# Kernel tuning notes

Hardware: AMD Instinct MI355X
Metric: run time of the kernel (lower is better)

The kernel has to match this reference:

```python
import jax, jax.numpy as jnp
import numpy as np

HIDDEN = 2048
N_HEADS = 16
N_KV_HEADS = 4
HEAD_DIM = HIDDEN // N_HEADS  # 128
ROPE_THETA = 10000.0
BATCH = 2
SEQ = 2048


def setup_inputs() -> dict:
    key = jax.random.key(0)
    k1, k2, k3, k4, k5 = jax.random.split(key, 5)
    s = 0.02
    return {
        "hidden_states": jax.random.normal(k1, (BATCH, SEQ, HIDDEN), dtype=jnp.float32),
        "attention_mask": jnp.zeros((BATCH, 1, 1, SEQ), dtype=jnp.float32),
        "Wq": jax.random.normal(k2, (HIDDEN, N_HEADS * HEAD_DIM), dtype=jnp.float32) * s,
        "Wk": jax.random.normal(k3, (HIDDEN, N_KV_HEADS * HEAD_DIM), dtype=jnp.float32) * s,
        "Wv": jax.random.normal(k4, (HIDDEN, N_KV_HEADS * HEAD_DIM), dtype=jnp.float32) * s,
        "Wo": jax.random.normal(k5, (N_HEADS * HEAD_DIM, HIDDEN), dtype=jnp.float32) * s,
    }


def _rope_cos_sin(seq_len, dtype):
    inv_freq = 1.0 / (ROPE_THETA ** (jnp.arange(0, HEAD_DIM, 2, dtype=jnp.float32) / HEAD_DIM))
    t = jnp.arange(seq_len, dtype=jnp.float32)
    freqs = t[:, None] * inv_freq[None, :]            # [S, D/2]
    emb = jnp.concatenate([freqs, freqs], axis=-1)    # [S, D]
    cos = jnp.cos(emb)[None, None, :, :].astype(dtype)  # [1,1,S,D]
    sin = jnp.sin(emb)[None, None, :, :].astype(dtype)
    return cos, sin


def _apply_rope(x, cos, sin):
    # x: [B,H,S,D]; faithful to torch code: rotated = cat((-x[...,1::2], x[...,::2]), -1)
    x1 = x[..., ::2]
    x2 = x[..., 1::2]
    rotated = jnp.concatenate([-x2, x1], axis=-1)
    return x * cos + rotated * sin


def reference(hidden_states, attention_mask, Wq, Wk, Wv, Wo):
    B, S, _ = hidden_states.shape
    scale = HEAD_DIM ** -0.5

    q = (hidden_states @ Wq).reshape(B, S, N_HEADS, HEAD_DIM).transpose(0, 2, 1, 3)      # [B,H,S,D]
    k = (hidden_states @ Wk).reshape(B, S, N_KV_HEADS, HEAD_DIM).transpose(0, 2, 1, 3)   # [B,KV,S,D]
    v = (hidden_states @ Wv).reshape(B, S, N_KV_HEADS, HEAD_DIM).transpose(0, 2, 1, 3)

    cos, sin = _rope_cos_sin(S, hidden_states.dtype)
    q = _apply_rope(q, cos, sin)
    k = _apply_rope(k, cos, sin)

    rep = N_HEADS // N_KV_HEADS
    k = jnp.repeat(k, rep, axis=1)  # [B,H,S,D]
    v = jnp.repeat(v, rep, axis=1)

    scores = jnp.einsum("bhqd,bhkd->bhqk", q, k) * scale  # [B,H,S,S]
    causal = jnp.tril(jnp.ones((S, S), dtype=bool))[None, None]
    scores = jnp.where(causal, scores, -jnp.inf)
    scores = scores + attention_mask  # additive float mask, broadcast [B,1,1,S]

    attn = jax.nn.softmax(scores, axis=-1)
    out = jnp.einsum("bhqk,bhkd->bhqd", attn, v)           # [B,H,S,D]
    out = out.transpose(0, 2, 1, 3).reshape(B, S, N_HEADS * HEAD_DIM)
    return out @ Wo
```

## Files before the change

### kernel.cpp

```cpp
#include <hip/hip_runtime.h>
#include <hip/hip_bf16.h>

#define BATCH 2
#define SEQ   2048
#define NH    16
#define NKV   4
#define HD    128
#define KDIM  2048
#define MROWS 4096
#define NQKV  3072

typedef __attribute__((ext_vector_type(8))) short  s16x8;
typedef __attribute__((ext_vector_type(4))) short  s16x4;
typedef __attribute__((ext_vector_type(4))) float  f32x4;
typedef __attribute__((ext_vector_type(8))) __bf16 b16x8;

__device__ __forceinline__ unsigned short f2bf(float f) {
  __hip_bfloat16 h = __float2bfloat16(f);
  return *reinterpret_cast<unsigned short*>(&h);
}
__device__ __forceinline__ float bf2f(unsigned short h) {
  union { unsigned int u; float f; } x; x.u = ((unsigned int)h) << 16;
  return x.f;
}

__device__ __forceinline__ f32x4 MFMA16(s16x8 a, s16x8 b, f32x4 c) {
  return __builtin_amdgcn_mfma_f32_16x16x32_bf16(
      __builtin_bit_cast(b16x8, a), __builtin_bit_cast(b16x8, b), c, 0, 0, 0);
}

__device__ __forceinline__ void gload_lds16(const void* g, void* lds) {
  __builtin_amdgcn_global_load_lds(
      (const __attribute__((address_space(1))) void*)g,
      (__attribute__((address_space(3))) void*)lds, 16, 0, 0);
}

__global__ __launch_bounds__(256) void transpose_convert(
    const float* __restrict__ W, unsigned short* __restrict__ WT, int Kd, int Nd) {
  __shared__ float tile[32][33];
  int n0 = blockIdx.x * 32, k0 = blockIdx.y * 32;
  int tx = threadIdx.x & 31, ty = threadIdx.x >> 5;
#pragma unroll
  for (int i = 0; i < 4; ++i)
    tile[ty + i * 8][tx] = W[(size_t)(k0 + ty + i * 8) * Nd + n0 + tx];
  __syncthreads();
#pragma unroll
  for (int i = 0; i < 4; ++i)
    WT[(size_t)(n0 + ty + i * 8) * Kd + k0 + tx] = f2bf(tile[tx][ty + i * 8]);
}

__global__ __launch_bounds__(256) void conv_bf16(
    const float* __restrict__ X, unsigned short* __restrict__ Y) {
  int i = blockIdx.x * 256 + threadIdx.x;
  const float4 a = ((const float4*)X)[2 * i];
  const float4 b = ((const float4*)X)[2 * i + 1];
  s16x8 o;
  o[0] = (short)f2bf(a.x); o[1] = (short)f2bf(a.y);
  o[2] = (short)f2bf(a.z); o[3] = (short)f2bf(a.w);
  o[4] = (short)f2bf(b.x); o[5] = (short)f2bf(b.y);
  o[6] = (short)f2bf(b.z); o[7] = (short)f2bf(b.w);
  ((s16x8*)Y)[i] = o;
}

__global__ __launch_bounds__(256) void rope_table_kernel(float* __restrict__ tbl) {
  int i = blockIdx.x * 256 + threadIdx.x;
  int s = i >> 6, j = i & 63;
  float inv = powf(10000.0f, -(float)(2 * j) * (1.0f / 128.0f));
  float f = (float)s * inv;
  tbl[2 * i]     = cosf(f);
  tbl[2 * i + 1] = sinf(f);
}

__global__ __launch_bounds__(256) void gemm_qkv(
    const unsigned short* __restrict__ A, const unsigned short* __restrict__ BT,
    unsigned short* __restrict__ Qo, unsigned short* __restrict__ Ko,
    unsigned short* __restrict__ Vo) {
  __shared__ __align__(16) unsigned short la[128][32];
  __shared__ __align__(16) unsigned short lb[128][32];
  int tid = threadIdx.x, lane = tid & 63, w = tid >> 6;
  int m0 = blockIdx.y * 128, n0 = blockIdx.x * 128;
  int wr = (w >> 1) * 64, wc = (w & 1) * 64;
  int fr = lane & 15, kg = (lane >> 4) * 8, rg = (lane >> 4) * 4;
  f32x4 acc[4][4] = {};
  for (int kt = 0; kt < KDIM; kt += 32) {
    __syncthreads();
#pragma unroll
    for (int i = 0; i < 2; ++i) {
      int idx = tid + i * 256;
      int row = idx >> 2, seg = idx & 3;
      gload_lds16(A + (size_t)(m0 + row) * KDIM + kt + seg * 8,
                  (char*)la + (size_t)(i * 256 + w * 64) * 16);
      gload_lds16(BT + (size_t)(n0 + row) * KDIM + kt + seg * 8,
                  (char*)lb + (size_t)(i * 256 + w * 64) * 16);
    }
    __syncthreads();
    s16x8 af[4], bf[4];
#pragma unroll
    for (int mi = 0; mi < 4; ++mi) af[mi] = *(const s16x8*)(&la[wr + mi * 16 + fr][kg]);
#pragma unroll
    for (int ni = 0; ni < 4; ++ni) bf[ni] = *(const s16x8*)(&lb[wc + ni * 16 + fr][kg]);
#pragma unroll
    for (int mi = 0; mi < 4; ++mi)
#pragma unroll
      for (int ni = 0; ni < 4; ++ni) acc[mi][ni] = MFMA16(af[mi], bf[ni], acc[mi][ni]);
  }
  int rbase = m0 + wr + rg;
#pragma unroll
  for (int ni = 0; ni < 4; ++ni) {
    int gn = n0 + wc + ni * 16 + fr;
    if (gn < 2048) {
      int hh = gn >> 7, d = gn & 127;
#pragma unroll
      for (int mi = 0; mi < 4; ++mi)
#pragma unroll
        for (int r = 0; r < 4; ++r) {
          int grow = rbase + mi * 16 + r;
          int bb = grow >> 11, ss = grow & 2047;
          Qo[((size_t)(bb * NH + hh) * SEQ + ss) * HD + d] = f2bf(acc[mi][ni][r]);
        }
    } else if (gn < 2560) {
      int c = gn - 2048, kvh = c >> 7, d = c & 127;
#pragma unroll
      for (int mi = 0; mi < 4; ++mi)
#pragma unroll
        for (int r = 0; r < 4; ++r) {
          int grow = rbase + mi * 16 + r;
          int bb = grow >> 11, ss = grow & 2047;
          Ko[((size_t)(bb * NKV + kvh) * SEQ + ss) * HD + d] = f2bf(acc[mi][ni][r]);
        }
    } else {
      int c = gn - 2560, kvh = c >> 7, d = c & 127;
#pragma unroll
      for (int mi = 0; mi < 4; ++mi) {
        int grow0 = rbase + mi * 16;
        int bb = grow0 >> 11, ss = grow0 & 2047;
        s16x4 pk;
#pragma unroll
        for (int r = 0; r < 4; ++r) pk[r] = (short)f2bf(acc[mi][ni][r]);
        *(s16x4*)(Vo + ((size_t)(bb * NKV + kvh) * HD + d) * SEQ + ss) = pk;
      }
    }
  }
}

__global__ __launch_bounds__(256) void gemm_out(
    const unsigned short* __restrict__ A, const unsigned short* __restrict__ BT,
    float* __restrict__ C) {
  __shared__ __align__(16) unsigned short la[128][32];
  __shared__ __align__(16) unsigned short lb[128][32];
  int tid = threadIdx.x, lane = tid & 63, w = tid >> 6;
  int m0 = blockIdx.y * 128, n0 = blockIdx.x * 128;
  int wr = (w >> 1) * 64, wc = (w & 1) * 64;
  int fr = lane & 15, kg = (lane >> 4) * 8, rg = (lane >> 4) * 4;
  f32x4 acc[4][4] = {};
  for (int kt = 0; kt < KDIM; kt += 32) {
    __syncthreads();
#pragma unroll
    for (int i = 0; i < 2; ++i) {
      int idx = tid + i * 256;
      int row = idx >> 2, seg = idx & 3;
      gload_lds16(A + (size_t)(m0 + row) * KDIM + kt + seg * 8,
                  (char*)la + (size_t)(i * 256 + w * 64) * 16);
      gload_lds16(BT + (size_t)(n0 + row) * KDIM + kt + seg * 8,
                  (char*)lb + (size_t)(i * 256 + w * 64) * 16);
    }
    __syncthreads();
    s16x8 af[4], bf[4];
#pragma unroll
    for (int mi = 0; mi < 4; ++mi) af[mi] = *(const s16x8*)(&la[wr + mi * 16 + fr][kg]);
#pragma unroll
    for (int ni = 0; ni < 4; ++ni) bf[ni] = *(const s16x8*)(&lb[wc + ni * 16 + fr][kg]);
#pragma unroll
    for (int mi = 0; mi < 4; ++mi)
#pragma unroll
      for (int ni = 0; ni < 4; ++ni) acc[mi][ni] = MFMA16(af[mi], bf[ni], acc[mi][ni]);
  }
  int rbase = m0 + wr + rg;
#pragma unroll
  for (int ni = 0; ni < 4; ++ni) {
    int gn = n0 + wc + ni * 16 + fr;
#pragma unroll
    for (int mi = 0; mi < 4; ++mi)
#pragma unroll
      for (int r = 0; r < 4; ++r)
        C[(size_t)(rbase + mi * 16 + r) * 2048 + gn] = acc[mi][ni][r];
  }
}

__global__ __launch_bounds__(256) void rope2(
    unsigned short* __restrict__ X, const float* __restrict__ tbl) {
  __shared__ __align__(16) unsigned short xs[32][136];
  int tid = threadIdx.x;
  size_t r0 = (size_t)blockIdx.x * 32;
#pragma unroll
  for (int i = 0; i < 2; ++i) {
    int idx = tid + i * 256;
    int pr = idx >> 4, seg = idx & 15;
    *(s16x8*)(&xs[pr][seg * 8]) = *(const s16x8*)(X + (r0 + pr) * 128 + seg * 8);
  }
  __syncthreads();
  int pr = tid >> 3, jb = (tid & 7) * 8;
  size_t row = r0 + pr;
  int s = (int)(row & (SEQ - 1));
  s16x8 o0, o1;
#pragma unroll
  for (int j0 = 0; j0 < 8; ++j0) {
    int j = jb + j0;
    float c  = tbl[(s * 64 + j) * 2];
    float sn = tbl[(s * 64 + j) * 2 + 1];
    float xj   = bf2f(xs[pr][j]);
    float xj64 = bf2f(xs[pr][j + 64]);
    float x2j  = bf2f(xs[pr][2 * j]);
    float x2j1 = bf2f(xs[pr][2 * j + 1]);
    o0[j0] = (short)f2bf(xj * c - x2j1 * sn);
    o1[j0] = (short)f2bf(xj64 * c + x2j * sn);
  }
  unsigned short* xp = X + row * 128;
  *(s16x8*)(xp + jb)      = o0;
  *(s16x8*)(xp + 64 + jb) = o1;
}

__global__ __launch_bounds__(512, 2) void attn_fwd(
    const unsigned short* __restrict__ Q, const unsigned short* __restrict__ K,
    const unsigned short* __restrict__ VT, const float* __restrict__ mask,
    unsigned short* __restrict__ O) {
  __shared__ __align__(16) unsigned short kt_[2][64][136];
  __shared__ __align__(16) unsigned short vt_[128][68];
  __shared__ __align__(16) unsigned short pt_[8][16][36];

  int tid = threadIdx.x, lane = tid & 63, w = tid >> 6;
  int l = blockIdx.x;
  int grp = l & 7, slot = l >> 3;
  int hloc = slot & 3, p = slot >> 2;
  int b = grp >> 2, kvh = grp & 3, h = kvh * 4 + hloc;
  int half = w >> 2, wsub = w & 3;
  int qt = half ? p : 31 - p;
  int qw = qt * 64 + wsub * 16;
  int fr = lane & 15, g = lane >> 4, kg = g * 8, rg = g * 4;

  const unsigned short* Qb = Q + (size_t)(b * NH + h) * SEQ * HD;
  const unsigned short* Kb = K + (size_t)(b * NKV + kvh) * SEQ * HD;
  const unsigned short* Vb = VT + (size_t)(b * NKV + kvh) * HD * SEQ;
  const float* mb = mask + (size_t)b * SEQ;

  int krow = tid >> 4, kpos = (tid & 15) * 8;
  int vrow = tid >> 3, vcol = (tid & 7) * 8;

  const float sc2 = 0.12751744584812722f;
  const float L2E = 1.44269504088896f;
  int bS = b * SEQ;
  int ntiles = 32 - p;

  s16x8 aq[4];
#pragma unroll
  for (int dc = 0; dc < 4; ++dc)
    aq[dc] = *(const s16x8*)(Qb + (size_t)(qw + fr) * HD + dc * 32 + kg);

  f32x4 oacc[8] = {};
  float m_r = -3e38f, l_r = 0.f;

  s16x8 kreg[2], vreg[2];
  kreg[0] = *(const s16x8*)(Kb + (size_t)krow * HD + kpos);
  kreg[1] = *(const s16x8*)(Kb + (size_t)(krow + 32) * HD + kpos);
  vreg[0] = *(const s16x8*)(Vb + (size_t)vrow * SEQ + vcol);
  vreg[1] = *(const s16x8*)(Vb + (size_t)(vrow + 64) * SEQ + vcol);
  *(s16x8*)(&kt_[0][krow][kpos])      = kreg[0];
  *(s16x8*)(&kt_[0][krow + 32][kpos]) = kreg[1];
  __syncthreads();

  int cur = 0;
  for (int t = 0; t < ntiles; ++t) {
    int kv0 = t * 64;
    bool notlast = (t + 1 < ntiles);
    bool active = (kv0 <= qw + 15);
    bool diag   = (kv0 + 63 > qw);

    *(s16x8*)(&vt_[vrow][vcol])      = vreg[0];
    *(s16x8*)(&vt_[vrow + 64][vcol]) = vreg[1];
    if (notlast) {
      kreg[0] = *(const s16x8*)(Kb + (size_t)(kv0 + 64 + krow) * HD + kpos);
      kreg[1] = *(const s16x8*)(Kb + (size_t)(kv0 + 96 + krow) * HD + kpos);
    }

    f32x4 sf[4];
    if (active) {
      __builtin_amdgcn_s_setprio(1);
#pragma unroll
      for (int mk = 0; mk < 4; ++mk) {
        s16x8 ak[4];
#pragma unroll
        for (int dc = 0; dc < 4; ++dc)
          ak[dc] = *(const s16x8*)(&kt_[cur][mk * 16 + fr][dc * 32 + kg]);
        sf[mk] = f32x4{0.f, 0.f, 0.f, 0.f};
#pragma unroll
        for (int dc = 0; dc < 4; ++dc)
          sf[mk] = MFMA16(ak[dc], aq[dc], sf[mk]);
      }
      __builtin_amdgcn_s_setprio(0);

#pragma unroll
      for (int mk = 0; mk < 4; ++mk) {
        float4 mv = *(const float4*)(mb + kv0 + mk * 16 + rg);
        float mvr[4] = {mv.x * L2E, mv.y * L2E, mv.z * L2E, mv.w * L2E};
        if (diag) {
#pragma unroll
          for (int r = 0; r < 4; ++r) {
            int kv = kv0 + mk * 16 + rg + r;
            float v = sf[mk][r] * sc2 + mvr[r];
            sf[mk][r] = (kv <= qw + fr) ? v : -3e38f;
          }
        } else {
#pragma unroll
          for (int r = 0; r < 4; ++r)
            sf[mk][r] = sf[mk][r] * sc2 + mvr[r];
        }
      }

      float pm = -3e38f;
#pragma unroll
      for (int mk = 0; mk < 4; ++mk)
#pragma unroll
        for (int r = 0; r < 4; ++r) pm = fmaxf(pm, sf[mk][r]);
      pm = fmaxf(pm, __shfl_xor(pm, 16, 64));
      pm = fmaxf(pm, __shfl_xor(pm, 32, 64));
      if (!__all(pm - m_r <= 8.0f)) {
        float mo = m_r;
        float mn = fmaxf(mo, pm);
        float al = exp2f(mo - mn);
        m_r = mn;
        l_r *= al;
#pragma unroll
        for (int r = 0; r < 4; ++r) {
          float ar = __shfl(al, rg + r, 16);
#pragma unroll
          for (int od = 0; od < 8; ++od) oacc[od][r] *= ar;
        }
      }
      float rs = 0.f;
#pragma unroll
      for (int mk = 0; mk < 4; ++mk)
#pragma unroll
        for (int r = 0; r < 4; ++r) {
          float ppv = exp2f(sf[mk][r] - m_r);
          sf[mk][r] = ppv;
          rs += ppv;
        }
      rs += __shfl_xor(rs, 16, 64);
      rs += __shfl_xor(rs, 32, 64);
      l_r += rs;
    }

    if (notlast) {
      *(s16x8*)(&kt_[cur ^ 1][krow][kpos])      = kreg[0];
      *(s16x8*)(&kt_[cur ^ 1][krow + 32][kpos]) = kreg[1];
    }
    __syncthreads();

    if (notlast) {
      vreg[0] = *(const s16x8*)(Vb + (size_t)vrow * SEQ + kv0 + 64 + vcol);
      vreg[1] = *(const s16x8*)(Vb + (size_t)(vrow + 64) * SEQ + kv0 + 64 + vcol);
    }

    if (active) {
#pragma unroll
      for (int kk = 0; kk < 2; ++kk) {
#pragma unroll
        for (int mh = 0; mh < 2; ++mh) {
          int mk = kk * 2 + mh;
          s16x4 pk;
#pragma unroll
          for (int r = 0; r < 4; ++r) pk[r] = (short)f2bf(sf[mk][r]);
          *(s16x4*)(&pt_[w][fr][mh * 16 + rg]) = pk;
        }
        s16x8 ap = *(const s16x8*)(&pt_[w][fr][kg]);
        __builtin_amdgcn_s_setprio(1);
#pragma unroll
        for (int od = 0; od < 8; ++od) {
          s16x8 bv = *(const s16x8*)(&vt_[od * 16 + fr][kk * 32 + kg]);
          oacc[od] = MFMA16(ap, bv, oacc[od]);
        }
        __builtin_amdgcn_s_setprio(0);
      }
    }
    __syncthreads();
    cur ^= 1;
  }

  float iv = 1.0f / l_r;
  float ivr[4];
#pragma unroll
  for (int r = 0; r < 4; ++r) ivr[r] = __shfl(iv, rg + r, 16);
#pragma unroll
  for (int r = 0; r < 4; ++r) {
    unsigned short* op = O + (size_t)(bS + qw + rg + r) * 2048 + h * 128 + fr;
#pragma unroll
    for (int od = 0; od < 8; ++od)
      op[od * 16] = f2bf(oacc[od][r] * ivr[r]);
  }
}

extern "C" void kernel_launch(void* const* d_in, const int* in_sizes, int n_in,
                              void* d_out, int out_size, void* d_ws, size_t ws_size,
                              hipStream_t stream) {
  const float* hidden = (const float*)d_in[0];
  const float* mask   = (const float*)d_in[1];
  const float* Wq     = (const float*)d_in[2];
  const float* Wk     = (const float*)d_in[3];
  const float* Wv     = (const float*)d_in[4];
  const float* Wo     = (const float*)d_in[5];
  float* out = (float*)d_out;

  char* ws = (char*)d_ws;
  unsigned short* BT  = (unsigned short*)(ws);
  unsigned short* WoT = (unsigned short*)(ws + 12582912);
  unsigned short* Qb  = (unsigned short*)(ws + 20971520);
  unsigned short* Kb  = (unsigned short*)(ws + 37748736);
  unsigned short* VT  = (unsigned short*)(ws + 41943040);
  unsigned short* AO  = (unsigned short*)(ws + 46137344);
  float*          tbl = (float*)(ws + 62914560);
  unsigned short* Ab  = AO;

  conv_bf16<<<MROWS * KDIM / (256 * 8), 256, 0, stream>>>(hidden, Ab);
  transpose_convert<<<dim3(64, 64), 256, 0, stream>>>(Wq, BT, KDIM, 2048);
  transpose_convert<<<dim3(16, 64), 256, 0, stream>>>(Wk, BT + (size_t)2048 * KDIM, KDIM, 512);
  transpose_convert<<<dim3(16, 64), 256, 0, stream>>>(Wv, BT + (size_t)2560 * KDIM, KDIM, 512);
  transpose_convert<<<dim3(64, 64), 256, 0, stream>>>(Wo, WoT, KDIM, 2048);
  rope_table_kernel<<<512, 256, 0, stream>>>(tbl);

  gemm_qkv<<<dim3(NQKV / 128, MROWS / 128), 256, 0, stream>>>(Ab, BT, Qb, Kb, VT);
  rope2<<<(BATCH * NH * SEQ) / 32, 256, 0, stream>>>(Qb, tbl);
  rope2<<<(BATCH * NKV * SEQ) / 32, 256, 0, stream>>>(Kb, tbl);
  attn_fwd<<<dim3(512), 512, 0, stream>>>(Qb, Kb, VT, mask, AO);
  gemm_out<<<dim3(2048 / 128, MROWS / 128), 256, 0, stream>>>(AO, WoT, out);
}
```

Measured before the change: 229.8 us.

## Swizzle GEMM block order, use LDS-only barriers, tree-reduce row max

Both GEMMs now launch on a 1D grid and remap block indices with an XCD-aware swizzle, so consecutive blocks on the same XCD work on nearby tiles and share L2. The attention kernel replaces __syncthreads with a barrier that waits only for LDS counters, so outstanding global prefetch loads of K/V need not drain at each barrier. The row-max reduction becomes a balanced tree to shorten the dependency chain. These are three separate changes; if the barrier ordering assumption is wrong, the weaker barrier could cause a race.

Result: no change. 230.9 us (+0.5%).

```diff
diff --git a/kernel.cpp b/kernel.cpp
--- a/kernel.cpp
+++ b/kernel.cpp
@@ -14,6 +14,11 @@
 typedef __attribute__((ext_vector_type(4))) short  s16x4;
 typedef __attribute__((ext_vector_type(4))) float  f32x4;
 typedef __attribute__((ext_vector_type(8))) __bf16 b16x8;
+
+#define BARRIER_LDS() do { \
+    asm volatile("s_waitcnt lgkmcnt(0)" ::: "memory"); \
+    __builtin_amdgcn_s_barrier(); \
+  } while (0)
 
 __device__ __forceinline__ unsigned short f2bf(float f) {
   __hip_bfloat16 h = __float2bfloat16(f);
@@ -78,7 +83,10 @@
   __shared__ __align__(16) unsigned short la[128][32];
   __shared__ __align__(16) unsigned short lb[128][32];
   int tid = threadIdx.x, lane = tid & 63, w = tid >> 6;
-  int m0 = blockIdx.y * 128, n0 = blockIdx.x * 128;
+  int lin = blockIdx.x;
+  int swz = (lin & 7) * 96 + (lin >> 3);
+  int bx = swz % 24, by = swz / 24;
+  int m0 = by * 128, n0 = bx * 128;
   int wr = (w >> 1) * 64, wc = (w & 1) * 64;
   int fr = lane & 15, kg = (lane >> 4) * 8, rg = (lane >> 4) * 4;
   f32x4 acc[4][4] = {};
@@ -149,7 +157,10 @@
   __shared__ __align__(16) unsigned short la[128][32];
   __shared__ __align__(16) unsigned short lb[128][32];
   int tid = threadIdx.x, lane = tid & 63, w = tid >> 6;
-  int m0 = blockIdx.y * 128, n0 = blockIdx.x * 128;
+  int lin = blockIdx.x;
+  int swz = (lin & 7) * 64 + (lin >> 3);
+  int bx = swz % 16, by = swz / 16;
+  int m0 = by * 128, n0 = bx * 128;
   int wr = (w >> 1) * 64, wc = (w & 1) * 64;
   int fr = lane & 15, kg = (lane >> 4) * 8, rg = (lane >> 4) * 4;
   f32x4 acc[4][4] = {};
@@ -266,7 +277,7 @@
   vreg[1] = *(const s16x8*)(Vb + (size_t)(vrow + 64) * SEQ + vcol);
   *(s16x8*)(&kt_[0][krow][kpos])      = kreg[0];
   *(s16x8*)(&kt_[0][krow + 32][kpos]) = kreg[1];
-  __syncthreads();
+  BARRIER_LDS();
 
   int cur = 0;
   for (int t = 0; t < ntiles; ++t) {
@@ -316,11 +327,13 @@
         }
       }
 
-      float pm = -3e38f;
-#pragma unroll
-      for (int mk = 0; mk < 4; ++mk)
-#pragma unroll
-        for (int r = 0; r < 4; ++r) pm = fmaxf(pm, sf[mk][r]);
+      float pm01a = fmaxf(sf[0][0], sf[0][1]), pm01b = fmaxf(sf[0][2], sf[0][3]);
+      float pm11a = fmaxf(sf[1][0], sf[1][1]), pm11b = fmaxf(sf[1][2], sf[1][3]);
+      float pm21a = fmaxf(sf[2][0], sf[2][1]), pm21b = fmaxf(sf[2][2], sf[2][3]);
+      float pm31a = fmaxf(sf[3][0], sf[3][1]), pm31b = fmaxf(sf[3][2], sf[3][3]);
+      float pm0 = fmaxf(pm01a, pm01b), pm1 = fmaxf(pm11a, pm11b);
+      float pm2 = fmaxf(pm21a, pm21b), pm3 = fmaxf(pm31a, pm31b);
+      float pm = fmaxf(fmaxf(pm0, pm1), fmaxf(pm2, pm3));
       pm = fmaxf(pm, __shfl_xor(pm, 16, 64));
       pm = fmaxf(pm, __shfl_xor(pm, 32, 64));
       if (!__all(pm - m_r <= 8.0f)) {
@@ -354,7 +367,7 @@
       *(s16x8*)(&kt_[cur ^ 1][krow][kpos])      = kreg[0];
       *(s16x8*)(&kt_[cur ^ 1][krow + 32][kpos]) = kreg[1];
     }
-    __syncthreads();
+    BARRIER_LDS();
 
     if (notlast) {
       vreg[0] = *(const s16x8*)(Vb + (size_t)vrow * SEQ + kv0 + 64 + vcol);
@@ -382,7 +395,7 @@
         __builtin_amdgcn_s_setprio(0);
       }
     }
-    __syncthreads();
+    BARRIER_LDS();
     cur ^= 1;
   }
 
@@ -427,9 +440,9 @@
   transpose_convert<<<dim3(64, 64), 256, 0, stream>>>(Wo, WoT, KDIM, 2048);
   rope_table_kernel<<<512, 256, 0, stream>>>(tbl);
 
-  gemm_qkv<<<dim3(NQKV / 128, MROWS / 128), 256, 0, stream>>>(Ab, BT, Qb, Kb, VT);
+  gemm_qkv<<<dim3(768), 256, 0, stream>>>(Ab, BT, Qb, Kb, VT);
   rope2<<<(BATCH * NH * SEQ) / 32, 256, 0, stream>>>(Qb, tbl);
   rope2<<<(BATCH * NKV * SEQ) / 32, 256, 0, stream>>>(Kb, tbl);
   attn_fwd<<<dim3(512), 512, 0, stream>>>(Qb, Kb, VT, mask, AO);
-  gemm_out<<<dim3(2048 / 128, MROWS / 128), 256, 0, stream>>>(AO, WoT, out);
-}
+  gemm_out<<<dim3(512), 256, 0, stream>>>(AO, WoT, out);
+}
```
